# Performance work log

Hardware: AMD Instinct MI355X
Metric: run time of the kernel (lower is better)

## Reference

```python
import jax, jax.numpy as jnp
import numpy as np

K_QUERY = 3    # opt.k: each point assigned to its 3 nearest SOM nodes
SOM_K = 9      # opt.som_k: 3x3 SOM neighborhood
EPS = 1e-5


def _lin1d(w, b, h):
    # 1x1 conv1d + relu: h is B,Cin,N
    return jax.nn.relu(jnp.einsum('oi,bin->bon', w, h) + b[None, :, None])


def _lin2d(w, b, h):
    # 1x1 conv2d + relu: h is B,Cin,M,K
    return jax.nn.relu(jnp.einsum('oi,bimk->bomk', w, h) + b[None, :, None, None])


def _gather_nb(feat, I):
    # feat: B,C,M ; I: B,M,K (node indices) -> B,C,M,K
    B, C, M = feat.shape
    K = I.shape[2]
    idx = jnp.broadcast_to(I[:, None, :, :], (B, C, M, K))
    return jnp.take_along_axis(feat[:, :, :, None], idx, axis=2)


def setup_inputs():
    key = jax.random.key(0)
    B, N, M = 8, 8192, 64
    ks = jax.random.split(key, 16)
    def w(k, o, i):
        return (jax.random.normal(k, (o, i), jnp.float32) / np.sqrt(i).astype(np.float32))
    return {
        'x': jax.random.normal(ks[0], (B, 3, N), jnp.float32),
        'sn': jax.random.normal(ks[1], (B, 3, N), jnp.float32),
        'node': jax.random.normal(ks[2], (B, 3, M), jnp.float32),
        'node_knn_I': jax.random.randint(ks[3], (B, M, SOM_K), 0, M),
        # PointResNet(6, [64,128,256,384])
        'pr_w0': w(ks[4], 64, 6), 'pr_b0': jnp.zeros((64,), jnp.float32),
        'pr_w1': w(ks[5], 128, 64), 'pr_b1': jnp.zeros((128,), jnp.float32),
        'pr_w2': w(ks[6], 256, 128), 'pr_b2': jnp.zeros((256,), jnp.float32),
        'pr_w3': w(ks[7], 384, 64 + 256), 'pr_b3': jnp.zeros((384,), jnp.float32),
        # KNNModule(3+384, (512,512))
        'knn_w0': w(ks[8], 512, 3 + 384), 'knn_b0': jnp.zeros((512,), jnp.float32),
        'knn_w1': w(ks[9], 512, 512), 'knn_b1': jnp.zeros((512,), jnp.float32),
        # final PointNet(3+512, (768,1024))
        'fin_w0': w(ks[10], 768, 3 + 512), 'fin_b0': jnp.zeros((768,), jnp.float32),
        'fin_w1': w(ks[11], 1024, 768), 'fin_b1': jnp.zeros((1024,), jnp.float32),
    }


def reference(x, sn, node, node_knn_I, pr_w0, pr_b0, pr_w1, pr_b1, pr_w2, pr_b2,
              pr_w3, pr_b3, knn_w0, knn_b0, knn_w1, knn_b1, fin_w0, fin_b0,
              fin_w1, fin_b1):
    B, _, N = x.shape
    M = node.shape[2]
    k = K_QUERY
    kN = k * N
    # --- som.query_topk: assign each point to its k nearest SOM nodes ---
    xd = jax.lax.stop_gradient(x)
    dist = jnp.sum((node[:, :, :, None] - xd[:, :, None, :]) ** 2, axis=1)  # B,M,N
    _, idx = jax.lax.top_k(-jnp.swapaxes(dist, 1, 2), k)                     # B,N,k
    min_idx = jnp.transpose(idx, (0, 2, 1)).reshape(B, kN)                   # B,kN (k blocks of N)
    mask = jax.nn.one_hot(min_idx, M, dtype=x.dtype)                         # B,kN,M
    mask_row_sum = jnp.sum(mask, axis=1)                                     # B,M
    mask_row_max = jnp.max(mask, axis=1) > 0                                 # B,M
    x_stack = jnp.tile(x, (1, 1, k))                                         # B,3,kN
    sn_stack = jnp.tile(sn, (1, 1, k))
    # --- masked segment-mean -> per-node cluster centers (detached) ---
    cluster_mean = jax.lax.stop_gradient(
        jnp.einsum('bcn,bnm->bcm', x_stack, mask) / (mask_row_sum[:, None, :] + EPS))
    centers = jnp.einsum('bcm,bnm->bcn', cluster_mean, mask)                 # B,3,kN
    x_decentered = jax.lax.stop_gradient(x_stack - centers)
    x_aug = jnp.concatenate([x_decentered, sn_stack], axis=1)                # B,6,kN
    # --- PointResNet(6,[64,128,256,384]) ---
    h0 = _lin1d(pr_w0, pr_b0, x_aug)
    h1 = _lin1d(pr_w1, pr_b1, h0)
    h2 = _lin1d(pr_w2, pr_b2, h1)
    first = _lin1d(pr_w3, pr_b3, jnp.concatenate([h0, h2], axis=1))          # B,384,kN
    # --- index_max scatter-max: per-node per-channel max over assigned points ---
    seg = (min_idx + (jnp.arange(B)[:, None] * M)).reshape(-1)               # (B*kN,)
    data = jnp.transpose(first, (0, 2, 1)).reshape(B * kN, -1)               # (B*kN, C)
    node_max = jax.ops.segment_max(data, seg, num_segments=B * M)            # (B*M, C)
    node_max = jnp.transpose(node_max.reshape(B, M, -1), (0, 2, 1))          # B,C,M
    # empty nodes gather index 0 in the original (gather_index * mask_row_max)
    first_masked_max = jnp.where(mask_row_max[:, None, :], node_max, first[:, :, 0:1])
    # --- KNNModule over SOM nodes (som_k=9, 'avg' centering) ---
    coord_knn = _gather_nb(cluster_mean, node_knn_I)                         # B,3,M,K
    center = jnp.mean(coord_knn, axis=3)                                     # B,3,M
    feat_knn = _gather_nb(first_masked_max, node_knn_I)                      # B,384,M,K
    aug = jnp.concatenate([coord_knn - center[:, :, :, None], feat_knn], axis=1)
    g = _lin2d(knn_w1, knn_b1, _lin2d(knn_w0, knn_b0, aug))                  # B,512,M,K
    knn_feature = jnp.max(g, axis=3)                                         # B,512,M
    # --- final PointNet(3+512,(768,1024)) + global max pool ---
    f = _lin1d(fin_w1, fin_b1,
               _lin1d(fin_w0, fin_b0, jnp.concatenate([center, knn_feature], axis=1)))
    return jnp.max(f, axis=2)                                                # B,1024
```

## Files before the change

### kernel.cpp

```cpp
#include <hip/hip_runtime.h>

typedef unsigned short u16;
typedef unsigned int   u32;
typedef _Float16 f16;
typedef _Float16 f16x8 __attribute__((ext_vector_type(8)));
typedef _Float16 f16x4 __attribute__((ext_vector_type(4)));
typedef float    f32x4 __attribute__((ext_vector_type(4)));

#define BQ 8
#define NQ 8192
#define MQ 64
#define SEGS (BQ*MQ)
#define MAXCHUNK 3584
#define KBA 10
#define NCOLS_D 4608
#define ROWL 520

#define OFF_IDX      (size_t)0
#define OFF_PERM     (size_t)786432
#define OFF_CNT      (size_t)1572864
#define OFF_SUMS     (size_t)1574912
#define OFF_OFFS     (size_t)1581056
#define OFF_CURSOR   (size_t)1583360
#define OFF_NCHUNK   (size_t)1585408
#define OFF_CHUNKTAB (size_t)1585664
#define OFF_MEAN     (size_t)1614336
#define OFF_FALLBACK (size_t)1620480
#define OFF_NODEMAX  (size_t)1632768
#define OFF_CENTER   (size_t)2419200
#define OFF_W1P      (size_t)2425344
#define OFF_W2P      (size_t)2441728
#define OFF_W3P      (size_t)2507264
#define OFF_KNW0P    (size_t)2753024
#define OFF_KNW1P    (size_t)3179008
#define OFF_FINW0P   (size_t)3703296
#define OFF_FINW1P   (size_t)4538880
#define OFF_AUG      (size_t)6111744
#define OFF_MID1     (size_t)9945600
#define OFF_GBUF     (size_t)14664192
#define OFF_KEIN     (size_t)19382784
#define OFF_MIDE     (size_t)19939840

__device__ __forceinline__ void wpack(const float* __restrict__ W, f16* __restrict__ out,
                                      int K, int KB, int NF, int idx) {
  int e  = idx & 7;
  int l  = (idx >> 3) & 63;
  int kb = (idx >> 9) % KB;
  int rt = idx / (KB << 9);
  int row = rt * 16 + (l & 15);
  int c = kb * 32 + ((l >> 4) << 3) + e;
  int oc;
  if (NF < 0) oc = (c < K) ? c : -1;
  else        oc = (c < NF) ? (3 + c) : ((c < NF + 3) ? (c - NF) : -1);
  out[idx] = (oc >= 0) ? (f16)W[row * K + oc] : (f16)0.f;
}
__global__ __launch_bounds__(256) void kW(
    const float* pr_w1, const float* pr_w2, const float* pr_w3,
    const float* knn_w0, const float* knn_w1, const float* fin_w0, const float* fin_w1,
    f16* w1p, f16* w2p, f16* w3p, f16* knw0p, f16* knw1p, f16* finw0p, f16* finw1p) {
  int blk = blockIdx.x;
  int t = threadIdx.x;
  if (blk < 32)        wpack(pr_w1,  w1p,   64,  2, -1, blk * 256 + t);
  else if (blk < 160)  wpack(pr_w2,  w2p,  128,  4, -1, (blk - 32) * 256 + t);
  else if (blk < 640)  wpack(pr_w3,  w3p,  320, 10, -1, (blk - 160) * 256 + t);
  else if (blk < 1472) wpack(knn_w0, knw0p, 387, 13, 384, (blk - 640) * 256 + t);
  else if (blk < 2496) wpack(knn_w1, knw1p, 512, 16, -1, (blk - 1472) * 256 + t);
  else if (blk < 4128) wpack(fin_w0, finw0p, 515, 17, 512, (blk - 2496) * 256 + t);
  else                 wpack(fin_w1, finw1p, 768, 24, -1, (blk - 4128) * 256 + t);
}

__global__ __launch_bounds__(256) void kA(const float* __restrict__ x, const float* __restrict__ node,
                                          int* __restrict__ idx_buf, int* __restrict__ cnt,
                                          float* __restrict__ sums) {
#pragma clang fp contract(off)
  __shared__ float ns[3][64];
  __shared__ int cbin[64];
  __shared__ float sbin[3][64];
  int b = blockIdx.y;
  int t = threadIdx.x;
  if (t < 192) { int c = t >> 6, m = t & 63; ns[c][m] = node[(b * 3 + c) * 64 + m]; }
  if (t < 64) { cbin[t] = 0; sbin[0][t] = 0.f; sbin[1][t] = 0.f; sbin[2][t] = 0.f; }
  __syncthreads();
  int n = blockIdx.x * 256 + t;
  float x0 = x[(b * 3 + 0) * NQ + n];
  float x1 = x[(b * 3 + 1) * NQ + n];
  float x2 = x[(b * 3 + 2) * NQ + n];
  float d0 = 3.4e38f, d1 = 3.4e38f, d2 = 3.4e38f;
  int i0 = 0, i1 = 0, i2 = 0;
  for (int m = 0; m < 64; ++m) {
    float da = ns[0][m] - x0;
    float db = ns[1][m] - x1;
    float dc = ns[2][m] - x2;
    float d = da * da + db * db + dc * dc;
    if (d < d0)      { d2 = d1; i2 = i1; d1 = d0; i1 = i0; d0 = d; i0 = m; }
    else if (d < d1) { d2 = d1; i2 = i1; d1 = d;  i1 = m; }
    else if (d < d2) { d2 = d;  i2 = m; }
  }
  int base = (b * NQ + n) * 3;
  idx_buf[base + 0] = i0; idx_buf[base + 1] = i1; idx_buf[base + 2] = i2;
  int ms[3] = {i0, i1, i2};
  #pragma unroll
  for (int j = 0; j < 3; ++j) {
    int m = ms[j];
    atomicAdd(&cbin[m], 1);
    atomicAdd(&sbin[0][m], x0);
    atomicAdd(&sbin[1][m], x1);
    atomicAdd(&sbin[2][m], x2);
  }
  __syncthreads();
  if (t < 64 && cbin[t] > 0) {
    atomicAdd(&cnt[b * 64 + t], cbin[t]);
    atomicAdd(&sums[(b * 64 + t) * 3 + 0], sbin[0][t]);
    atomicAdd(&sums[(b * 64 + t) * 3 + 1], sbin[1][t]);
    atomicAdd(&sums[(b * 64 + t) * 3 + 2], sbin[2][t]);
  }
}

__global__ __launch_bounds__(256) void kB(const int* __restrict__ cnt, const float* __restrict__ sums,
                                          int* __restrict__ offs, int* __restrict__ cursor,
                                          int* __restrict__ nchunks, int* __restrict__ chunk_tab,
                                          float* __restrict__ mean, const int* __restrict__ knn_I,
                                          float* __restrict__ centerb) {
  __shared__ int sps[256], spc[256];
  int t = threadIdx.x;
  int c0 = cnt[2 * t], c1 = cnt[2 * t + 1];
  sps[t] = c0 + c1;
  spc[t] = ((c0 + 63) >> 6) + ((c1 + 63) >> 6);
  __syncthreads();
  for (int d = 1; d < 256; d <<= 1) {
    int a = 0, q = 0;
    if (t >= d) { a = sps[t - d]; q = spc[t - d]; }
    __syncthreads();
    if (t >= d) { sps[t] += a; spc[t] += q; }
    __syncthreads();
  }
  int pbase = t ? sps[t - 1] : 0;
  int cbase = t ? spc[t - 1] : 0;
  offs[2 * t] = pbase;        offs[2 * t + 1] = pbase + c0;
  cursor[2 * t] = pbase;      cursor[2 * t + 1] = pbase + c0;
  if (t == 255) { offs[512] = sps[255]; nchunks[0] = spc[255]; }
  int st = pbase, ci = cbase, s = 2 * t, c = c0;
  #pragma unroll
  for (int rep = 0; rep < 2; ++rep) {
    while (c > 0) {
      int l = c > 64 ? 64 : c;
      chunk_tab[2 * ci] = (s << 16) | l;
      chunk_tab[2 * ci + 1] = st;
      st += l; c -= l; ++ci;
    }
    s = 2 * t + 1; c = c1; st = pbase + c0;
  }
  for (int i = t; i < SEGS * 3; i += 256) mean[i] = sums[i] / ((float)cnt[i / 3] + 1e-5f);
  for (int seg = t; seg < SEGS; seg += 256) {
    int b = seg >> 6;
    float s0 = 0.f, s1 = 0.f, s2 = 0.f;
    for (int kk = 0; kk < 9; ++kk) {
      int q = b * 64 + knn_I[seg * 9 + kk];
      float inv = 1.f / ((float)cnt[q] + 1e-5f);
      s0 += sums[q * 3 + 0] * inv;
      s1 += sums[q * 3 + 1] * inv;
      s2 += sums[q * 3 + 2] * inv;
    }
    centerb[seg * 3 + 0] = s0 * (1.f / 9.f);
    centerb[seg * 3 + 1] = s1 * (1.f / 9.f);
    centerb[seg * 3 + 2] = s2 * (1.f / 9.f);
  }
}

__global__ __launch_bounds__(256) void kA2(const int* __restrict__ idx_buf, int* __restrict__ cursor,
                                           int* __restrict__ perm) {
  __shared__ int loc[64];
  __shared__ int base_s[64];
  int b = blockIdx.y;
  int t = threadIdx.x;
  if (t < 64) loc[t] = 0;
  __syncthreads();
  int n = blockIdx.x * 256 + t;
  int base = (b * NQ + n) * 3;
  int m0 = idx_buf[base + 0], m1 = idx_buf[base + 1], m2 = idx_buf[base + 2];
  int l0 = atomicAdd(&loc[m0], 1);
  int l1 = atomicAdd(&loc[m1], 1);
  int l2 = atomicAdd(&loc[m2], 1);
  __syncthreads();
  if (t < 64 && loc[t] > 0) base_s[t] = atomicAdd(&cursor[b * 64 + t], loc[t]);
  __syncthreads();
  perm[base_s[m0] + l0] = (b << 21) | (n << 8) | (0 << 6) | m0;
  perm[base_s[m1] + l1] = (b << 21) | (n << 8) | (1 << 6) | m1;
  perm[base_s[m2] + l2] = (b << 21) | (n << 8) | (2 << 6) | m2;
}

__global__ __launch_bounds__(512, 2) void kC(
    const float* __restrict__ x, const float* __restrict__ sn,
    const float* __restrict__ mean, const int* __restrict__ perm,
    const int* __restrict__ chunk_tab, const int* __restrict__ nchunks,
    const float* __restrict__ w0, const float* __restrict__ b0v,
    const f16* __restrict__ w1p, const float* __restrict__ b1v,
    const f16* __restrict__ w2p, const float* __restrict__ b2v,
    const f16* __restrict__ w3p, const float* __restrict__ b3v,
    float* __restrict__ node_max, float* __restrict__ fallback) {
  __shared__ __align__(16) f16 bufA[4 * KBA * ROWL];
  __shared__ __align__(16) f16 bufH1[4 * 4 * ROWL];
  __shared__ float in_s[6][64];
  __shared__ float w0_s[448];
  __shared__ float b3_s[384];
  __shared__ int flag_s[64];
  __shared__ int n_s[64];
  int tid = threadIdx.x;
  int wid  = __builtin_amdgcn_readfirstlane(tid >> 6);
  int lane = tid & 63;
  int pcol = lane & 15;
  int g    = lane >> 4;

  for (int i = tid; i < 384; i += 512) { w0_s[i] = w0[i]; b3_s[i] = b3v[i]; }
  if (tid < 64) w0_s[384 + tid] = b0v[tid];

  f16x8 af2h[2];
  #pragma unroll
  for (int kb = 0; kb < 2; ++kb)
    af2h[kb] = *(const f16x8*)(w1p + (size_t)((wid * 2 + kb) * 64 + lane) * 8);
  f16x8 af4h[3][KBA];
  #pragma unroll
  for (int c = 0; c < 3; ++c)
    #pragma unroll
    for (int kb = 0; kb < KBA; ++kb)
      af4h[c][kb] = *(const f16x8*)(w3p + (size_t)(((wid * 3 + c) * KBA + kb) * 64 + lane) * 8);

  int nch = nchunks[0];
  for (int blk = blockIdx.x; blk < nch; blk += gridDim.x) {
    __syncthreads();
    int e0    = chunk_tab[2 * blk];
    int start = chunk_tab[2 * blk + 1];
    int seg = e0 >> 16, len = e0 & 0xffff;
    int b = seg >> 6;
    if (tid < 64) {
      int n = 0, fl = 0;
      if (tid < len) {
        int rec = perm[start + tid];
        n = (rec >> 8) & 0x1fff;
        fl = (n == 0 && (((rec >> 6) & 3) == 0)) ? 1 : 0;
      }
      n_s[tid] = n;
      flag_s[tid] = fl;
    }
    __syncthreads();
    {
      int p = tid >> 3, c = tid & 7;
      if (c < 6) {
        int n = n_s[p];
        float v;
        if (c < 3) v = x[((size_t)b * 3 + c) * NQ + n] - mean[seg * 3 + c];
        else       v = sn[((size_t)b * 3 + (c - 3)) * NQ + n];
        in_s[c][p] = v;
      }
    }
    f16x8 af3[2][4];
    #pragma unroll
    for (int s = 0; s < 2; ++s)
      #pragma unroll
      for (int kb = 0; kb < 4; ++kb)
        af3[s][kb] = *(const f16x8*)(w2p + (size_t)(((wid * 2 + s) * 4 + kb) * 64 + lane) * 8);
    __syncthreads();

    {
      float a0 = in_s[0][lane], a1 = in_s[1][lane], a2 = in_s[2][lane];
      float a3 = in_s[3][lane], a4 = in_s[4][lane], a5 = in_s[5][lane];
      f16x8 v;
      #pragma unroll
      for (int i = 0; i < 8; ++i) {
        const float* wr = &w0_s[(wid * 8 + i) * 6];
        float s = w0_s[384 + wid * 8 + i];
        s = fmaf(wr[0], a0, s); s = fmaf(wr[1], a1, s); s = fmaf(wr[2], a2, s);
        s = fmaf(wr[3], a3, s); s = fmaf(wr[4], a4, s); s = fmaf(wr[5], a5, s);
        v[i] = (f16)fmaxf(s, 0.f);
      }
      int kb = wid >> 2, q = wid & 3;
      *(f16x8*)&bufA[(g * KBA + kb) * ROWL + (pcol + 16 * q) * 8] = v;
    }
    __syncthreads();

    f32x4 acc1[4] = {};
    #pragma unroll
    for (int kb = 0; kb < 2; ++kb) {
      #pragma unroll
      for (int pt = 0; pt < 4; ++pt) {
        f16x8 bf = *(const f16x8*)&bufA[(pt * KBA + kb) * ROWL + lane * 8];
        acc1[pt] = __builtin_amdgcn_mfma_f32_16x16x32_f16(af2h[kb], bf, acc1[pt], 0, 0, 0);
      }
    }
    {
      float4 bb = *(const float4*)&b1v[wid * 16 + g * 4];
      int kbo = wid >> 1;
      int q   = ((wid & 1) << 1) + (g >> 1);
      int ee  = (g & 1) * 4;
      #pragma unroll
      for (int pt = 0; pt < 4; ++pt) {
        f16x4 v;
        v[0] = (f16)fmaxf(acc1[pt][0] + bb.x, 0.f);
        v[1] = (f16)fmaxf(acc1[pt][1] + bb.y, 0.f);
        v[2] = (f16)fmaxf(acc1[pt][2] + bb.z, 0.f);
        v[3] = (f16)fmaxf(acc1[pt][3] + bb.w, 0.f);
        *(f16x4*)&bufH1[(pt * 4 + kbo) * ROWL + (pcol + 16 * q) * 8 + ee] = v;
      }
    }
    __syncthreads();

    f32x4 acc2[2][4] = {};
    #pragma unroll
    for (int kb = 0; kb < 4; ++kb) {
      #pragma unroll
      for (int pt = 0; pt < 4; ++pt) {
        f16x8 bf = *(const f16x8*)&bufH1[(pt * 4 + kb) * ROWL + lane * 8];
        acc2[0][pt] = __builtin_amdgcn_mfma_f32_16x16x32_f16(af3[0][kb], bf, acc2[0][pt], 0, 0, 0);
        acc2[1][pt] = __builtin_amdgcn_mfma_f32_16x16x32_f16(af3[1][kb], bf, acc2[1][pt], 0, 0, 0);
      }
    }
    {
      int kbo = 2 + wid;
      #pragma unroll
      for (int s = 0; s < 2; ++s) {
        float4 bb = *(const float4*)&b2v[(wid * 2 + s) * 16 + g * 4];
        int q  = 2 * s + (g >> 1);
        int ee = (g & 1) * 4;
        #pragma unroll
        for (int pt = 0; pt < 4; ++pt) {
          f16x4 v;
          v[0] = (f16)fmaxf(acc2[s][pt][0] + bb.x, 0.f);
          v[1] = (f16)fmaxf(acc2[s][pt][1] + bb.y, 0.f);
          v[2] = (f16)fmaxf(acc2[s][pt][2] + bb.z, 0.f);
          v[3] = (f16)fmaxf(acc2[s][pt][3] + bb.w, 0.f);
          *(f16x4*)&bufA[(pt * KBA + kbo) * ROWL + (pcol + 16 * q) * 8 + ee] = v;
        }
      }
    }
    __syncthreads();

    f32x4 acc3[3][4] = {};
    #pragma unroll
    for (int kb = 0; kb < KBA; ++kb) {
      #pragma unroll
      for (int pt = 0; pt < 4; ++pt) {
        f16x8 bf = *(const f16x8*)&bufA[(pt * KBA + kb) * ROWL + lane * 8];
        acc3[0][pt] = __builtin_amdgcn_mfma_f32_16x16x32_f16(af4h[0][kb], bf, acc3[0][pt], 0, 0, 0);
        acc3[1][pt] = __builtin_amdgcn_mfma_f32_16x16x32_f16(af4h[1][kb], bf, acc3[1][pt], 0, 0, 0);
        acc3[2][pt] = __builtin_amdgcn_mfma_f32_16x16x32_f16(af4h[2][kb], bf, acc3[2][pt], 0, 0, 0);
      }
    }
    {
      int fl[4], vld[4];
      #pragma unroll
      for (int pt = 0; pt < 4; ++pt) {
        fl[pt]  = flag_s[pt * 16 + pcol];
        vld[pt] = (pt * 16 + pcol) < len;
      }
      #pragma unroll
      for (int c = 0; c < 3; ++c) {
        int ct = wid * 3 + c;
        #pragma unroll
        for (int j = 0; j < 4; ++j) {
          float bj = b3_s[ct * 16 + g * 4 + j];
          float vm = 0.f;
          #pragma unroll
          for (int pt = 0; pt < 4; ++pt) {
            float v = fmaxf(acc3[c][pt][j] + bj, 0.f);
            if (fl[pt]) fallback[b * 384 + ct * 16 + g * 4 + j] = v;
            if (!vld[pt]) v = 0.f;
            vm = fmaxf(vm, v);
          }
          vm = fmaxf(vm, __shfl_xor(vm, 1));
          vm = fmaxf(vm, __shfl_xor(vm, 2));
          vm = fmaxf(vm, __shfl_xor(vm, 4));
          vm = fmaxf(vm, __shfl_xor(vm, 8));
          if (pcol == 0)
            atomicMax((int*)&node_max[(size_t)seg * 384 + ct * 16 + g * 4 + j],
                      __float_as_int(vm));
        }
      }
    }
  }
}

__global__ __launch_bounds__(256) void kDg(
    const float* __restrict__ mean, const float* __restrict__ node_max,
    const float* __restrict__ fallback, const int* __restrict__ cnt,
    const int* __restrict__ knn_I, const float* __restrict__ centerb,
    f16* __restrict__ augP) {
  int idx = blockIdx.x * 256 + threadIdx.x;
  if (idx < NCOLS_D * 48) {
    int col = idx / 48;
    int rg  = idx - col * 48;
    int kk = col >> 9, seg = col & 511, b = seg >> 6;
    int nb = knn_I[seg * 9 + kk];
    const float* src = (cnt[b * 64 + nb] > 0) ? (node_max + (size_t)(b * 64 + nb) * 384)
                                              : (fallback + (size_t)b * 384);
    int r = rg * 8;
    f16x8 v;
    #pragma unroll
    for (int e = 0; e < 8; ++e) v[e] = (f16)src[r + e];
    int ct = col >> 4, pc = col & 15;
    int kb = r >> 5, ks = (r >> 3) & 3;
    *(f16x8*)&augP[(size_t)((ct * 13 + kb) * 64 + pc + 16 * ks) * 8] = v;
  } else if (idx < NCOLS_D * 48 + NCOLS_D) {
    int col = idx - NCOLS_D * 48;
    int kk = col >> 9, seg = col & 511, b = seg >> 6;
    int nb = knn_I[seg * 9 + kk];
    f16x8 v = {};
    #pragma unroll
    for (int c = 0; c < 3; ++c)
      v[c] = (f16)(mean[(b * 64 + nb) * 3 + c] - centerb[seg * 3 + c]);
    int ct = col >> 4, pc = col & 15;
    *(f16x8*)&augP[(size_t)((ct * 13 + 12) * 64 + pc) * 8] = v;
    f16x8 z = {};
    #pragma unroll
    for (int ks = 1; ks < 4; ++ks)
      *(f16x8*)&augP[(size_t)((ct * 13 + 12) * 64 + pc + 16 * ks) * 8] = z;
  }
}

template<int NKB_IN, int NKB_OUT, int MODE>
__global__ __launch_bounds__(256) void kGemm(
    const f16* __restrict__ Ap, const f16* __restrict__ Bp,
    const float* __restrict__ bias, f16* __restrict__ outP, float* __restrict__ outF) {
  int cb = blockIdx.x;
  int rb = blockIdx.y;
  int tid = threadIdx.x;
  int wid = __builtin_amdgcn_readfirstlane(tid >> 6);
  int lane = tid & 63;
  int rt = rb * 4 + wid;
  f32x4 acc[4] = {};
  const f16* ap = Ap + (size_t)rt * NKB_IN * 512;
  const f16* bp = Bp + (size_t)cb * 4 * NKB_IN * 512;
  #pragma unroll
  for (int kb = 0; kb < NKB_IN; ++kb) {
    f16x8 af = *(const f16x8*)(ap + (size_t)(kb * 64 + lane) * 8);
    #pragma unroll
    for (int ct = 0; ct < 4; ++ct) {
      f16x8 bf = *(const f16x8*)(bp + (size_t)((ct * NKB_IN + kb) * 64 + lane) * 8);
      acc[ct] = __builtin_amdgcn_mfma_f32_16x16x32_f16(af, bf, acc[ct], 0, 0, 0);
    }
  }
  int pcol = lane & 15, g = lane >> 4;
  float4 bb = *(const float4*)&bias[rt * 16 + g * 4];
  float bj[4] = {bb.x, bb.y, bb.z, bb.w};
  if (MODE == 0) {
    int k0 = rt * 16 + g * 4;
    int kb2 = k0 >> 5, ks2 = (k0 >> 3) & 3, ee = k0 & 7;
    #pragma unroll
    for (int ct = 0; ct < 4; ++ct) {
      f16x4 v;
      #pragma unroll
      for (int j = 0; j < 4; ++j) v[j] = (f16)fmaxf(acc[ct][j] + bj[j], 0.f);
      int ctc = cb * 4 + ct;
      *(f16x4*)&outP[(size_t)((ctc * NKB_OUT + kb2) * 64 + pcol + 16 * ks2) * 8 + ee] = v;
    }
  } else if (MODE == 1) {
    #pragma unroll
    for (int ct = 0; ct < 4; ++ct) {
      f16x4 v;
      #pragma unroll
      for (int j = 0; j < 4; ++j) v[j] = (f16)fmaxf(acc[ct][j] + bj[j], 0.f);
      int col = cb * 64 + ct * 16 + pcol;
      *(f16x4*)&outP[(size_t)col * 512 + rt * 16 + g * 4] = v;
    }
  } else {
    #pragma unroll
    for (int j = 0; j < 4; ++j) {
      float v = fmaxf(acc[0][j] + bj[j], 0.f);
      #pragma unroll
      for (int ct = 1; ct < 4; ++ct) v = fmaxf(v, fmaxf(acc[ct][j] + bj[j], 0.f));
      v = fmaxf(v, __shfl_xor(v, 1));
      v = fmaxf(v, __shfl_xor(v, 2));
      v = fmaxf(v, __shfl_xor(v, 4));
      v = fmaxf(v, __shfl_xor(v, 8));
      if (pcol == 0) outF[cb * 1024 + rt * 16 + g * 4 + j] = v;
    }
  }
}

__global__ __launch_bounds__(256) void kDmax(const f16* __restrict__ gbuf,
                                             const float* __restrict__ centerb,
                                             f16* __restrict__ keinP) {
  int idx = blockIdx.x * 256 + threadIdx.x;
  if (idx < SEGS * 64) {
    int seg = idx >> 6;
    int rg  = idx & 63;
    int r = rg * 8;
    float m[8] = {};
    for (int kk = 0; kk < 9; ++kk) {
      f16x8 gv = *(const f16x8*)&gbuf[(size_t)(kk * 512 + seg) * 512 + r];
      #pragma unroll
      for (int e = 0; e < 8; ++e) m[e] = fmaxf(m[e], (float)gv[e]);
    }
    f16x8 v;
    #pragma unroll
    for (int e = 0; e < 8; ++e) v[e] = (f16)m[e];
    int ct = seg >> 4, pc = seg & 15;
    int kb = r >> 5, ks = (r >> 3) & 3;
    *(f16x8*)&keinP[(size_t)((ct * 17 + kb) * 64 + pc + 16 * ks) * 8] = v;
  } else if (idx < SEGS * 64 + SEGS) {
    int seg = idx - SEGS * 64;
    f16x8 v = {};
    #pragma unroll
    for (int c = 0; c < 3; ++c) v[c] = (f16)centerb[seg * 3 + c];
    int ct = seg >> 4, pc = seg & 15;
    *(f16x8*)&keinP[(size_t)((ct * 17 + 16) * 64 + pc) * 8] = v;
    f16x8 z = {};
    #pragma unroll
    for (int ks = 1; ks < 4; ++ks)
      *(f16x8*)&keinP[(size_t)((ct * 17 + 16) * 64 + pc + 16 * ks) * 8] = z;
  }
}

extern "C" void kernel_launch(void* const* d_in, const int* in_sizes, int n_in,
                              void* d_out, int out_size, void* d_ws, size_t ws_size,
                              hipStream_t stream) {
  const float* x      = (const float*)d_in[0];
  const float* sn     = (const float*)d_in[1];
  const float* node   = (const float*)d_in[2];
  const int*   knn_I  = (const int*)d_in[3];
  const float* pr_w0  = (const float*)d_in[4];
  const float* pr_b0  = (const float*)d_in[5];
  const float* pr_w1  = (const float*)d_in[6];
  const float* pr_b1  = (const float*)d_in[7];
  const float* pr_w2  = (const float*)d_in[8];
  const float* pr_b2  = (const float*)d_in[9];
  const float* pr_w3  = (const float*)d_in[10];
  const float* pr_b3  = (const float*)d_in[11];
  const float* knn_w0 = (const float*)d_in[12];
  const float* knn_b0 = (const float*)d_in[13];
  const float* knn_w1 = (const float*)d_in[14];
  const float* knn_b1 = (const float*)d_in[15];
  const float* fin_w0 = (const float*)d_in[16];
  const float* fin_b0 = (const float*)d_in[17];
  const float* fin_w1 = (const float*)d_in[18];
  const float* fin_b1 = (const float*)d_in[19];
  float* out = (float*)d_out;
  char* ws = (char*)d_ws;

  int*   idx_buf   = (int*)(ws + OFF_IDX);
  int*   perm      = (int*)(ws + OFF_PERM);
  int*   cnt       = (int*)(ws + OFF_CNT);
  float* sums      = (float*)(ws + OFF_SUMS);
  int*   offs      = (int*)(ws + OFF_OFFS);
  int*   cursor    = (int*)(ws + OFF_CURSOR);
  int*   nchunks   = (int*)(ws + OFF_NCHUNK);
  int*   chunk_tab = (int*)(ws + OFF_CHUNKTAB);
  float* mean      = (float*)(ws + OFF_MEAN);
  float* fallback  = (float*)(ws + OFF_FALLBACK);
  float* node_max  = (float*)(ws + OFF_NODEMAX);
  float* centerb   = (float*)(ws + OFF_CENTER);
  f16*   w1p       = (f16*)(ws + OFF_W1P);
  f16*   w2p       = (f16*)(ws + OFF_W2P);
  f16*   w3p       = (f16*)(ws + OFF_W3P);
  f16*   knw0p     = (f16*)(ws + OFF_KNW0P);
  f16*   knw1p     = (f16*)(ws + OFF_KNW1P);
  f16*   finw0p    = (f16*)(ws + OFF_FINW0P);
  f16*   finw1p    = (f16*)(ws + OFF_FINW1P);
  f16*   augP      = (f16*)(ws + OFF_AUG);
  f16*   mid1P     = (f16*)(ws + OFF_MID1);
  f16*   gbuf      = (f16*)(ws + OFF_GBUF);
  f16*   keinP     = (f16*)(ws + OFF_KEIN);
  f16*   midEP     = (f16*)(ws + OFF_MIDE);

  hipMemsetAsync(ws + OFF_CNT, 0, 8192, stream);
  hipMemsetAsync(ws + OFF_NODEMAX, 0, (size_t)SEGS * 384 * 4, stream);

  kW<<<7200, 256, 0, stream>>>(pr_w1, pr_w2, pr_w3, knn_w0, knn_w1, fin_w0, fin_w1,
                               w1p, w2p, w3p, knw0p, knw1p, finw0p, finw1p);

  dim3 gA(NQ / 256, BQ);
  kA<<<gA, 256, 0, stream>>>(x, node, idx_buf, cnt, sums);
  kB<<<1, 256, 0, stream>>>(cnt, sums, offs, cursor, nchunks, chunk_tab, mean, knn_I, centerb);
  kA2<<<gA, 256, 0, stream>>>(idx_buf, cursor, perm);
  kC<<<256, 512, 0, stream>>>(x, sn, mean, perm, chunk_tab, nchunks,
                              pr_w0, pr_b0, w1p, pr_b1, w2p, pr_b2, w3p, pr_b3,
                              node_max, fallback);
  kDg<<<(NCOLS_D * 48 + NCOLS_D + 255) / 256, 256, 0, stream>>>(
      mean, node_max, fallback, cnt, knn_I, centerb, augP);
  kGemm<13, 16, 0><<<dim3(72, 8), 256, 0, stream>>>(knw0p, augP, knn_b0, mid1P, nullptr);
  kGemm<16, 0, 1><<<dim3(72, 8), 256, 0, stream>>>(knw1p, mid1P, knn_b1, gbuf, nullptr);
  kDmax<<<(SEGS * 64 + SEGS + 255) / 256, 256, 0, stream>>>(gbuf, centerb, keinP);
  kGemm<17, 24, 0><<<dim3(8, 12), 256, 0, stream>>>(finw0p, keinP, fin_b0, midEP, nullptr);
  kGemm<24, 0, 2><<<dim3(8, 16), 256, 0, stream>>>(finw1p, midEP, fin_b1, nullptr, out);
}
```

Measured before the change: 287.4 us.

## Fuse KNN max-pool into second KNN GEMM and double-buffer point staging

The second KNN GEMM now takes the max over the 9 neighbours in registers (kGemmMax9), so the full g buffer is never written and the separate kDmax kernel is gone. The center column of keinP is written in kB instead. kC prefetches the next chunk's inputs and flags into a second shared buffer while the current chunk computes, removes row padding from the shared arrays, and sets waves-per-eu through an attribute. The fused GEMM runs on a much smaller grid (64 blocks instead of 576), so parallelism drops, and the unpadded shared rows may add LDS bank conflicts.

```diff
diff --git a/kernel.cpp b/kernel.cpp
--- a/kernel.cpp
+++ b/kernel.cpp
@@ -14,7 +14,6 @@
 #define MAXCHUNK 3584
 #define KBA 10
 #define NCOLS_D 4608
-#define ROWL 520
 
 #define OFF_IDX      (size_t)0
 #define OFF_PERM     (size_t)786432
@@ -37,7 +36,6 @@
 #define OFF_FINW1P   (size_t)4538880
 #define OFF_AUG      (size_t)6111744
 #define OFF_MID1     (size_t)9945600
-#define OFF_GBUF     (size_t)14664192
 #define OFF_KEIN     (size_t)19382784
 #define OFF_MIDE     (size_t)19939840
 
@@ -120,7 +118,7 @@
                                           int* __restrict__ offs, int* __restrict__ cursor,
                                           int* __restrict__ nchunks, int* __restrict__ chunk_tab,
                                           float* __restrict__ mean, const int* __restrict__ knn_I,
-                                          float* __restrict__ centerb) {
+                                          float* __restrict__ centerb, f16* __restrict__ keinP) {
   __shared__ int sps[256], spc[256];
   int t = threadIdx.x;
   int c0 = cnt[2 * t], c1 = cnt[2 * t + 1];
@@ -161,9 +159,18 @@
       s1 += sums[q * 3 + 1] * inv;
       s2 += sums[q * 3 + 2] * inv;
     }
-    centerb[seg * 3 + 0] = s0 * (1.f / 9.f);
-    centerb[seg * 3 + 1] = s1 * (1.f / 9.f);
-    centerb[seg * 3 + 2] = s2 * (1.f / 9.f);
+    s0 *= (1.f / 9.f); s1 *= (1.f / 9.f); s2 *= (1.f / 9.f);
+    centerb[seg * 3 + 0] = s0;
+    centerb[seg * 3 + 1] = s1;
+    centerb[seg * 3 + 2] = s2;
+    int ct = seg >> 4, pc = seg & 15;
+    f16x8 cv = {};
+    cv[0] = (f16)s0; cv[1] = (f16)s1; cv[2] = (f16)s2;
+    *(f16x8*)&keinP[(size_t)((ct * 17 + 16) * 64 + pc) * 8] = cv;
+    f16x8 z = {};
+    #pragma unroll
+    for (int ks = 1; ks < 4; ++ks)
+      *(f16x8*)&keinP[(size_t)((ct * 17 + 16) * 64 + pc + 16 * ks) * 8] = z;
   }
 }
 
@@ -189,7 +196,9 @@
   perm[base_s[m2] + l2] = (b << 21) | (n << 8) | (2 << 6) | m2;
 }
 
-__global__ __launch_bounds__(512, 2) void kC(
+__global__ __launch_bounds__(512)
+__attribute__((amdgpu_waves_per_eu(2, 2)))
+void kC(
     const float* __restrict__ x, const float* __restrict__ sn,
     const float* __restrict__ mean, const int* __restrict__ perm,
     const int* __restrict__ chunk_tab, const int* __restrict__ nchunks,
@@ -198,18 +207,19 @@
     const f16* __restrict__ w2p, const float* __restrict__ b2v,
     const f16* __restrict__ w3p, const float* __restrict__ b3v,
     float* __restrict__ node_max, float* __restrict__ fallback) {
-  __shared__ __align__(16) f16 bufA[4 * KBA * ROWL];
-  __shared__ __align__(16) f16 bufH1[4 * 4 * ROWL];
-  __shared__ float in_s[6][64];
+  __shared__ __align__(16) f16 bufA[4 * KBA * 512];
+  __shared__ __align__(16) f16 bufH1[4 * 4 * 512];
+  __shared__ float in_s[2][6][64];
   __shared__ float w0_s[448];
   __shared__ float b3_s[384];
-  __shared__ int flag_s[64];
-  __shared__ int n_s[64];
+  __shared__ int flag_s[2][64];
   int tid = threadIdx.x;
   int wid  = __builtin_amdgcn_readfirstlane(tid >> 6);
   int lane = tid & 63;
   int pcol = lane & 15;
   int g    = lane >> 4;
+  int sp = tid >> 3;
+  int sc = tid & 7;
 
   for (int i = tid; i < 384; i += 512) { w0_s[i] = w0[i]; b3_s[i] = b3v[i]; }
   if (tid < 64) w0_s[384 + tid] = b0v[tid];
@@ -226,44 +236,50 @@
       af4h[c][kb] = *(const f16x8*)(w3p + (size_t)(((wid * 3 + c) * KBA + kb) * 64 + lane) * 8);
 
   int nch = nchunks[0];
-  for (int blk = blockIdx.x; blk < nch; blk += gridDim.x) {
-    __syncthreads();
-    int e0    = chunk_tab[2 * blk];
-    int start = chunk_tab[2 * blk + 1];
+
+  #define STAGE(cidx, bi) do {                                                        \
+    int e0_ = chunk_tab[2 * (cidx)];                                                  \
+    int st_ = chunk_tab[2 * (cidx) + 1];                                              \
+    int seg_ = e0_ >> 16, len_ = e0_ & 0xffff, b_ = seg_ >> 6;                        \
+    if (sc < 6) {                                                                     \
+      float v_ = 0.f;                                                                 \
+      if (sp < len_) {                                                                \
+        int rec_ = perm[st_ + sp];                                                    \
+        int n_ = (rec_ >> 8) & 0x1fff;                                                \
+        if (sc < 3) v_ = x[(b_ * 3 + sc) * NQ + n_] - mean[seg_ * 3 + sc];            \
+        else        v_ = sn[(b_ * 3 + (sc - 3)) * NQ + n_];                           \
+      }                                                                               \
+      in_s[bi][sc][sp] = v_;                                                          \
+    } else if (sc == 6) {                                                             \
+      int fl_ = 0;                                                                    \
+      if (sp < len_) {                                                                \
+        int rec_ = perm[st_ + sp];                                                    \
+        fl_ = ((((rec_ >> 8) & 0x1fff) == 0) && (((rec_ >> 6) & 3) == 0)) ? 1 : 0;    \
+      }                                                                               \
+      flag_s[bi][sp] = fl_;                                                           \
+    }                                                                                 \
+  } while (0)
+
+  if (blockIdx.x < nch) STAGE(blockIdx.x, 0);
+  __syncthreads();
+
+  int buf = 0;
+  for (int blk = blockIdx.x; blk < nch; blk += 256) {
+    int e0  = chunk_tab[2 * blk];
     int seg = e0 >> 16, len = e0 & 0xffff;
     int b = seg >> 6;
-    if (tid < 64) {
-      int n = 0, fl = 0;
-      if (tid < len) {
-        int rec = perm[start + tid];
-        n = (rec >> 8) & 0x1fff;
-        fl = (n == 0 && (((rec >> 6) & 3) == 0)) ? 1 : 0;
-      }
-      n_s[tid] = n;
-      flag_s[tid] = fl;
-    }
-    __syncthreads();
-    {
-      int p = tid >> 3, c = tid & 7;
-      if (c < 6) {
-        int n = n_s[p];
-        float v;
-        if (c < 3) v = x[((size_t)b * 3 + c) * NQ + n] - mean[seg * 3 + c];
-        else       v = sn[((size_t)b * 3 + (c - 3)) * NQ + n];
-        in_s[c][p] = v;
-      }
-    }
+    int nxt = blk + 256;
+    if (nxt < nch) STAGE(nxt, buf ^ 1);
     f16x8 af3[2][4];
     #pragma unroll
     for (int s = 0; s < 2; ++s)
       #pragma unroll
       for (int kb = 0; kb < 4; ++kb)
         af3[s][kb] = *(const f16x8*)(w2p + (size_t)(((wid * 2 + s) * 4 + kb) * 64 + lane) * 8);
-    __syncthreads();
 
     {
-      float a0 = in_s[0][lane], a1 = in_s[1][lane], a2 = in_s[2][lane];
-      float a3 = in_s[3][lane], a4 = in_s[4][lane], a5 = in_s[5][lane];
+      float a0 = in_s[buf][0][lane], a1 = in_s[buf][1][lane], a2 = in_s[buf][2][lane];
+      float a3 = in_s[buf][3][lane], a4 = in_s[buf][4][lane], a5 = in_s[buf][5][lane];
       f16x8 v;
       #pragma unroll
       for (int i = 0; i < 8; ++i) {
@@ -274,7 +290,7 @@
         v[i] = (f16)fmaxf(s, 0.f);
       }
       int kb = wid >> 2, q = wid & 3;
-      *(f16x8*)&bufA[(g * KBA + kb) * ROWL + (pcol + 16 * q) * 8] = v;
+      *(f16x8*)&bufA[(g * KBA + kb) * 512 + (pcol + 16 * q) * 8] = v;
     }
     __syncthreads();
 
@@ -283,7 +299,7 @@
     for (int kb = 0; kb < 2; ++kb) {
       #pragma unroll
       for (int pt = 0; pt < 4; ++pt) {
-        f16x8 bf = *(const f16x8*)&bufA[(pt * KBA + kb) * ROWL + lane * 8];
+        f16x8 bf = *(const f16x8*)&bufA[(pt * KBA + kb) * 512 + lane * 8];
         acc1[pt] = __builtin_amdgcn_mfma_f32_16x16x32_f16(af2h[kb], bf, acc1[pt], 0, 0, 0);
       }
     }
@@ -299,7 +315,7 @@
         v[1] = (f16)fmaxf(acc1[pt][1] + bb.y, 0.f);
         v[2] = (f16)fmaxf(acc1[pt][2] + bb.z, 0.f);
         v[3] = (f16)fmaxf(acc1[pt][3] + bb.w, 0.f);
-        *(f16x4*)&bufH1[(pt * 4 + kbo) * ROWL + (pcol + 16 * q) * 8 + ee] = v;
+        *(f16x4*)&bufH1[(pt * 4 + kbo) * 512 + (pcol + 16 * q) * 8 + ee] = v;
       }
     }
     __syncthreads();
@@ -309,7 +325,7 @@
     for (int kb = 0; kb < 4; ++kb) {
       #pragma unroll
       for (int pt = 0; pt < 4; ++pt) {
-        f16x8 bf = *(const f16x8*)&bufH1[(pt * 4 + kb) * ROWL + lane * 8];
+        f16x8 bf = *(const f16x8*)&bufH1[(pt * 4 + kb) * 512 + lane * 8];
         acc2[0][pt] = __builtin_amdgcn_mfma_f32_16x16x32_f16(af3[0][kb], bf, acc2[0][pt], 0, 0, 0);
         acc2[1][pt] = __builtin_amdgcn_mfma_f32_16x16x32_f16(af3[1][kb], bf, acc2[1][pt], 0, 0, 0);
       }
@@ -328,7 +344,7 @@
           v[1] = (f16)fmaxf(acc2[s][pt][1] + bb.y, 0.f);
           v[2] = (f16)fmaxf(acc2[s][pt][2] + bb.z, 0.f);
           v[3] = (f16)fmaxf(acc2[s][pt][3] + bb.w, 0.f);
-          *(f16x4*)&bufA[(pt * KBA + kbo) * ROWL + (pcol + 16 * q) * 8 + ee] = v;
+          *(f16x4*)&bufA[(pt * KBA + kbo) * 512 + (pcol + 16 * q) * 8 + ee] = v;
         }
       }
     }
@@ -339,7 +355,7 @@
     for (int kb = 0; kb < KBA; ++kb) {
       #pragma unroll
       for (int pt = 0; pt < 4; ++pt) {
-        f16x8 bf = *(const f16x8*)&bufA[(pt * KBA + kb) * ROWL + lane * 8];
+        f16x8 bf = *(const f16x8*)&bufA[(pt * KBA + kb) * 512 + lane * 8];
         acc3[0][pt] = __builtin_amdgcn_mfma_f32_16x16x32_f16(af4h[0][kb], bf, acc3[0][pt], 0, 0, 0);
         acc3[1][pt] = __builtin_amdgcn_mfma_f32_16x16x32_f16(af4h[1][kb], bf, acc3[1][pt], 0, 0, 0);
         acc3[2][pt] = __builtin_amdgcn_mfma_f32_16x16x32_f16(af4h[2][kb], bf, acc3[2][pt], 0, 0, 0);
@@ -349,7 +365,7 @@
       int fl[4], vld[4];
       #pragma unroll
       for (int pt = 0; pt < 4; ++pt) {
-        fl[pt]  = flag_s[pt * 16 + pcol];
+        fl[pt]  = flag_s[buf][pt * 16 + pcol];
         vld[pt] = (pt * 16 + pcol) < len;
       }
       #pragma unroll
@@ -376,7 +392,10 @@
         }
       }
     }
-  }
+    __syncthreads();
+    buf ^= 1;
+  }
+  #undef STAGE
 }
 
 __global__ __launch_bounds__(256) void kDg(
@@ -452,15 +471,6 @@
       int ctc = cb * 4 + ct;
       *(f16x4*)&outP[(size_t)((ctc * NKB_OUT + kb2) * 64 + pcol + 16 * ks2) * 8 + ee] = v;
     }
-  } else if (MODE == 1) {
-    #pragma unroll
-    for (int ct = 0; ct < 4; ++ct) {
-      f16x4 v;
-      #pragma unroll
-      for (int j = 0; j < 4; ++j) v[j] = (f16)fmaxf(acc[ct][j] + bj[j], 0.f);
-      int col = cb * 64 + ct * 16 + pcol;
-      *(f16x4*)&outP[(size_t)col * 512 + rt * 16 + g * 4] = v;
-    }
   } else {
     #pragma unroll
     for (int j = 0; j < 4; ++j) {
@@ -476,37 +486,53 @@
   }
 }
 
-__global__ __launch_bounds__(256) void kDmax(const f16* __restrict__ gbuf,
-                                             const float* __restrict__ centerb,
-                                             f16* __restrict__ keinP) {
-  int idx = blockIdx.x * 256 + threadIdx.x;
-  if (idx < SEGS * 64) {
-    int seg = idx >> 6;
-    int rg  = idx & 63;
-    int r = rg * 8;
-    float m[8] = {};
-    for (int kk = 0; kk < 9; ++kk) {
-      f16x8 gv = *(const f16x8*)&gbuf[(size_t)(kk * 512 + seg) * 512 + r];
-      #pragma unroll
-      for (int e = 0; e < 8; ++e) m[e] = fmaxf(m[e], (float)gv[e]);
-    }
-    f16x8 v;
-    #pragma unroll
-    for (int e = 0; e < 8; ++e) v[e] = (f16)m[e];
-    int ct = seg >> 4, pc = seg & 15;
-    int kb = r >> 5, ks = (r >> 3) & 3;
-    *(f16x8*)&keinP[(size_t)((ct * 17 + kb) * 64 + pc + 16 * ks) * 8] = v;
-  } else if (idx < SEGS * 64 + SEGS) {
-    int seg = idx - SEGS * 64;
-    f16x8 v = {};
-    #pragma unroll
-    for (int c = 0; c < 3; ++c) v[c] = (f16)centerb[seg * 3 + c];
-    int ct = seg >> 4, pc = seg & 15;
-    *(f16x8*)&keinP[(size_t)((ct * 17 + 16) * 64 + pc) * 8] = v;
-    f16x8 z = {};
-    #pragma unroll
-    for (int ks = 1; ks < 4; ++ks)
-      *(f16x8*)&keinP[(size_t)((ct * 17 + 16) * 64 + pc + 16 * ks) * 8] = z;
+template<int NKB_IN, int NKB_OUT>
+__global__ __launch_bounds__(256) void kGemmMax9(
+    const f16* __restrict__ Ap, const f16* __restrict__ Bp,
+    const float* __restrict__ bias, f16* __restrict__ outP) {
+  int cb = blockIdx.x;
+  int rb = blockIdx.y;
+  int tid = threadIdx.x;
+  int wid = __builtin_amdgcn_readfirstlane(tid >> 6);
+  int lane = tid & 63;
+  int rt = rb * 4 + wid;
+  f16x8 af[NKB_IN];
+  #pragma unroll
+  for (int kb = 0; kb < NKB_IN; ++kb)
+    af[kb] = *(const f16x8*)(Ap + (size_t)((rt * NKB_IN + kb) * 64 + lane) * 8);
+  f32x4 mx[4];
+  #pragma unroll
+  for (int ct = 0; ct < 4; ++ct)
+    #pragma unroll
+    for (int j = 0; j < 4; ++j) mx[ct][j] = -3.4e38f;
+  for (int kk = 0; kk < 9; ++kk) {
+    f32x4 acc[4] = {};
+    const f16* bp = Bp + (size_t)(kk * 32 + cb * 4) * NKB_IN * 512;
+    #pragma unroll
+    for (int kb = 0; kb < NKB_IN; ++kb) {
+      #pragma unroll
+      for (int ct = 0; ct < 4; ++ct) {
+        f16x8 bf = *(const f16x8*)(bp + (size_t)((ct * NKB_IN + kb) * 64 + lane) * 8);
+        acc[ct] = __builtin_amdgcn_mfma_f32_16x16x32_f16(af[kb], bf, acc[ct], 0, 0, 0);
+      }
+    }
+    #pragma unroll
+    for (int ct = 0; ct < 4; ++ct)
+      #pragma unroll
+      for (int j = 0; j < 4; ++j) mx[ct][j] = fmaxf(mx[ct][j], acc[ct][j]);
+  }
+  int pcol = lane & 15, g = lane >> 4;
+  float4 bb = *(const float4*)&bias[rt * 16 + g * 4];
+  float bj[4] = {bb.x, bb.y, bb.z, bb.w};
+  int k0 = rt * 16 + g * 4;
+  int kb2 = k0 >> 5, ks2 = (k0 >> 3) & 3, ee = k0 & 7;
+  #pragma unroll
+  for (int ct = 0; ct < 4; ++ct) {
+    f16x4 v;
+    #pragma unroll
+    for (int j = 0; j < 4; ++j) v[j] = (f16)fmaxf(mx[ct][j] + bj[j], 0.f);
+    int ctc = cb * 4 + ct;
+    *(f16x4*)&outP[(size_t)((ctc * NKB_OUT + kb2) * 64 + pcol + 16 * ks2) * 8 + ee] = v;
   }
 }
 
@@ -557,7 +583,6 @@
   f16*   finw1p    = (f16*)(ws + OFF_FINW1P);
   f16*   augP      = (f16*)(ws + OFF_AUG);
   f16*   mid1P     = (f16*)(ws + OFF_MID1);
-  f16*   gbuf      = (f16*)(ws + OFF_GBUF);
   f16*   keinP     = (f16*)(ws + OFF_KEIN);
   f16*   midEP     = (f16*)(ws + OFF_MIDE);
 
@@ -569,7 +594,8 @@
 
   dim3 gA(NQ / 256, BQ);
   kA<<<gA, 256, 0, stream>>>(x, node, idx_buf, cnt, sums);
-  kB<<<1, 256, 0, stream>>>(cnt, sums, offs, cursor, nchunks, chunk_tab, mean, knn_I, centerb);
+  kB<<<1, 256, 0, stream>>>(cnt, sums, offs, cursor, nchunks, chunk_tab, mean, knn_I,
+                            centerb, keinP);
   kA2<<<gA, 256, 0, stream>>>(idx_buf, cursor, perm);
   kC<<<256, 512, 0, stream>>>(x, sn, mean, perm, chunk_tab, nchunks,
                               pr_w0, pr_b0, w1p, pr_b1, w2p, pr_b2, w3p, pr_b3,
@@ -577,8 +603,7 @@
   kDg<<<(NCOLS_D * 48 + NCOLS_D + 255) / 256, 256, 0, stream>>>(
       mean, node_max, fallback, cnt, knn_I, centerb, augP);
   kGemm<13, 16, 0><<<dim3(72, 8), 256, 0, stream>>>(knw0p, augP, knn_b0, mid1P, nullptr);
-  kGemm<16, 0, 1><<<dim3(72, 8), 256, 0, stream>>>(knw1p, mid1P, knn_b1, gbuf, nullptr);
-  kDmax<<<(SEGS * 64 + SEGS + 255) / 256, 256, 0, stream>>>(gbuf, centerb, keinP);
+  kGemmMax9<16, 17><<<dim3(8, 8), 256, 0, stream>>>(knw1p, mid1P, knn_b1, keinP);
   kGemm<17, 24, 0><<<dim3(8, 12), 256, 0, stream>>>(finw0p, keinP, fin_b0, midEP, nullptr);
   kGemm<24, 0, 2><<<dim3(8, 16), 256, 0, stream>>>(finw1p, midEP, fin_b1, nullptr, out);
 }
```

Measured after the change: 404.5 us. +40.8%, slower.
